# Kernel optimization log

Measured on AMD Instinct MI355X. Metric: run time of the kernel, lower is better.

Reference implementation:

```python
import jax, jax.numpy as jnp
import numpy as np

def _binarize(x):
    # sign-binarize: -1 where x<0 else +1 (matches tf.where(inputs<0,-1.0,1.0))
    return jnp.where(x < 0, -1.0, 1.0).astype(jnp.float32)

def setup_inputs() -> dict:
    key = jax.random.key(0)
    k1, k2 = jax.random.split(key)
    B, D_IN, D_OUT = 8192, 4096, 4096
    inputs = jax.random.normal(k1, (B, D_IN), dtype=jnp.float32)
    # build() initializes kernel with RandomNormal(stddev=0.1) then assigns its binarized
    # version; we store the pre-binarized values since call() re-binarizes anyway.
    kernel = 0.1 * jax.random.normal(k2, (D_IN, D_OUT), dtype=jnp.float32)
    bias = jnp.zeros((D_OUT,), dtype=jnp.float32)
    return {"inputs": inputs, "kernel": kernel, "bias": bias}

def reference(inputs, kernel, bias):
    bx = _binarize(inputs)          # [B, D_in] in {-1, +1}
    bw = _binarize(kernel)          # [D_in, D_out] in {-1, +1}
    out = bx @ bw + bias            # [B, D_out]
    return jnp.tanh(out)
```

## Files before the change

### kernel.cpp

```cpp
#include <hip/hip_runtime.h>


#define B_DIM 8192
#define K_DIM 4096
#define N_DIM 4096
#define BK 64
#define NT (K_DIM / BK)

typedef int   i32x4 __attribute__((ext_vector_type(4)));
typedef unsigned char u8;

__device__ __forceinline__ unsigned char binq8(float v) {
    return (v < 0.0f) ? 0xFFu : 0x01u;
}

__device__ __forceinline__ float fast_tanh(float x) {
    float ax = __builtin_fabsf(x);
    float t  = __expf(-2.0f * ax);
    float r  = (1.0f - t) * __builtin_amdgcn_rcpf(1.0f + t);
    return __builtin_copysignf(r, x);
}

__global__ __launch_bounds__(256) void binarize_a_kernel(
    const float* __restrict__ in, u8* __restrict__ out, long n16) {
    long i = (long)blockIdx.x * blockDim.x + threadIdx.x;
    const long stride = (long)gridDim.x * blockDim.x;
    for (; i < n16; i += stride) {
        const float4* p = (const float4*)in + 4 * i;
        float4 v0 = p[0], v1 = p[1], v2 = p[2], v3 = p[3];
        unsigned int w0 = (unsigned)binq8(v0.x) | ((unsigned)binq8(v0.y) << 8)
                        | ((unsigned)binq8(v0.z) << 16) | ((unsigned)binq8(v0.w) << 24);
        unsigned int w1 = (unsigned)binq8(v1.x) | ((unsigned)binq8(v1.y) << 8)
                        | ((unsigned)binq8(v1.z) << 16) | ((unsigned)binq8(v1.w) << 24);
        unsigned int w2 = (unsigned)binq8(v2.x) | ((unsigned)binq8(v2.y) << 8)
                        | ((unsigned)binq8(v2.z) << 16) | ((unsigned)binq8(v2.w) << 24);
        unsigned int w3 = (unsigned)binq8(v3.x) | ((unsigned)binq8(v3.y) << 8)
                        | ((unsigned)binq8(v3.z) << 16) | ((unsigned)binq8(v3.w) << 24);
        i32x4 o = {(int)w0, (int)w1, (int)w2, (int)w3};
        *(i32x4*)(out + i * 16) = o;
    }
}

__global__ __launch_bounds__(256) void bintrans_kernel(
    const float* __restrict__ W, u8* __restrict__ Bt) {
    __shared__ u8 tile[64][64];
    const int n0  = blockIdx.x * 64;
    const int k0  = blockIdx.y * 64;
    const int tid = threadIdx.x;
    const int r   = tid >> 4;
    const int c4  = (tid & 15) * 4;
#pragma unroll
    for (int i = 0; i < 4; ++i) {
        const int k = i * 16 + r;
        float4 v = *(const float4*)(W + (size_t)(k0 + k) * N_DIM + n0 + c4);
        unsigned int p = (unsigned)binq8(v.x) | ((unsigned)binq8(v.y) << 8)
                       | ((unsigned)binq8(v.z) << 16) | ((unsigned)binq8(v.w) << 24);
        *(unsigned int*)&tile[k][c4] = p;
    }
    __syncthreads();
    const int n  = tid >> 2;
    const int ks = (tid & 3) * 16;
    unsigned int o[4];
#pragma unroll
    for (int q = 0; q < 4; ++q) {
        unsigned int p = 0;
#pragma unroll
        for (int j = 0; j < 4; ++j)
            p |= (unsigned)tile[ks + q * 4 + j][n] << (8 * j);
        o[q] = p;
    }
    i32x4 ov = {(int)o[0], (int)o[1], (int)o[2], (int)o[3]};
    *(i32x4*)(Bt + (size_t)(n0 + n) * K_DIM + k0 + ks) = ov;
}

__global__ __launch_bounds__(512, 2) void bgemm_kernel(
    const u8* __restrict__ A,
    const u8* __restrict__ Bt,
    const float* __restrict__ bias,
    float* __restrict__ C) {

    __shared__ __align__(1024) char lds[131072];

    const int tid = threadIdx.x;
    const int l   = tid & 63;
    const int w   = tid >> 6;
    const int wr  = w >> 2;
    const int wc  = w & 3;

    const int wg  = blockIdx.x;
    const int per = gridDim.x >> 3;
    const int swz = (wg & 7) * per + (wg >> 3);
    const int NBN = N_DIM / 256;
    const int bm  = swz / NBN;
    const int bn  = swz % NBN;

    const int sslot = (tid & 3) ^ ((tid >> 3) & 3);
    const u8* A0 = A  + (size_t)(bm * 256 + (tid >> 2)) * K_DIM + sslot * 16;
    const u8* B0 = Bt + (size_t)(bn * 256 + (tid >> 2)) * K_DIM + sslot * 16;
    const int ldsA_st = w * 1024;
    const int ldsB_st = 16384 + w * 1024;

    const int colb = ((l >> 4) ^ ((l >> 1) & 3)) << 4;
    const int aoff = (wr * 128 + (l & 15)) * 64 + colb;
    const int boff = 16384 + (wc * 64 + (l & 15)) * 64 + colb;

#define GLL(srcp, ldsoff)                                                        \
    __builtin_amdgcn_global_load_lds(                                            \
        (const __attribute__((address_space(1))) void*)(srcp),                   \
        (__attribute__((address_space(3))) void*)(lds + (ldsoff)), 16, 0, 0)

    i32x4 acc[8][4];
#pragma unroll
    for (int mf = 0; mf < 8; ++mf)
#pragma unroll
        for (int nf = 0; nf < 4; ++nf) acc[mf][nf] = (i32x4){0, 0, 0, 0};

#pragma unroll
    for (int tp = 0; tp < 3; ++tp) {
        const int db = tp << 15;
        const int kk = tp * BK;
        GLL(A0 + kk,                          db + ldsA_st);
        GLL(A0 + (size_t)128 * K_DIM + kk,    db + ldsA_st + 8192);
        GLL(B0 + kk,                          db + ldsB_st);
        GLL(B0 + (size_t)128 * K_DIM + kk,    db + ldsB_st + 8192);
    }
    asm volatile("s_waitcnt vmcnt(8)" ::: "memory");
    __builtin_amdgcn_s_barrier();

    for (int t = 0; t < NT; ++t) {
        const int cur = (t & 3) << 15;
        const int db  = ((t + 3) & 3) << 15;
        const int tp  = (t + 3 < NT) ? (t + 3) : 0;
        const int kk  = tp * BK;

        i32x4 a[4], b[4];

        GLL(A0 + kk,                       db + ldsA_st);
        GLL(A0 + (size_t)128 * K_DIM + kk, db + ldsA_st + 8192);
#pragma unroll
        for (int nf = 0; nf < 4; ++nf)
            b[nf] = *(const i32x4*)(lds + cur + boff + nf * 1024);
#pragma unroll
        for (int mf = 0; mf < 4; ++mf)
            a[mf] = *(const i32x4*)(lds + cur + aoff + mf * 1024);
        __builtin_amdgcn_s_barrier();
        asm volatile("s_waitcnt lgkmcnt(0)" ::: "memory");
        __builtin_amdgcn_sched_barrier(0);
        __builtin_amdgcn_s_setprio(1);
#pragma unroll
        for (int mf = 0; mf < 4; ++mf)
#pragma unroll
            for (int nf = 0; nf < 4; ++nf)
                acc[mf][nf] = __builtin_amdgcn_mfma_i32_16x16x64_i8(
                    a[mf], b[nf], acc[mf][nf], 0, 0, 0);
        __builtin_amdgcn_s_setprio(0);
        __builtin_amdgcn_s_barrier();

        GLL(B0 + kk,                       db + ldsB_st);
        GLL(B0 + (size_t)128 * K_DIM + kk, db + ldsB_st + 8192);
#pragma unroll
        for (int mf = 0; mf < 4; ++mf)
            a[mf] = *(const i32x4*)(lds + cur + aoff + 4096 + mf * 1024);
        __builtin_amdgcn_s_barrier();
        asm volatile("s_waitcnt lgkmcnt(0)" ::: "memory");
        __builtin_amdgcn_sched_barrier(0);
        __builtin_amdgcn_s_setprio(1);
#pragma unroll
        for (int mf = 0; mf < 4; ++mf)
#pragma unroll
            for (int nf = 0; nf < 4; ++nf)
                acc[4 + mf][nf] = __builtin_amdgcn_mfma_i32_16x16x64_i8(
                    a[mf], b[nf], acc[4 + mf][nf], 0, 0, 0);
        __builtin_amdgcn_s_setprio(0);
        asm volatile("s_waitcnt vmcnt(8)" ::: "memory");
        __builtin_amdgcn_s_barrier();
    }

    const int cn  = l & 15;
    const int cr4 = (l >> 4) * 4;
    float bv[4];
#pragma unroll
    for (int nf = 0; nf < 4; ++nf)
        bv[nf] = bias[bn * 256 + wc * 64 + nf * 16 + cn];

#pragma unroll
    for (int mf = 0; mf < 8; ++mf) {
        const size_t row0 = (size_t)bm * 256 + wr * 128 + mf * 16 + cr4;
#pragma unroll
        for (int nf = 0; nf < 4; ++nf) {
            const size_t col = (size_t)bn * 256 + wc * 64 + nf * 16 + cn;
#pragma unroll
            for (int r = 0; r < 4; ++r)
                C[(row0 + r) * N_DIM + col] =
                    fast_tanh((float)acc[mf][nf][r] + bv[nf]);
        }
    }
#undef GLL
}

extern "C" void kernel_launch(void* const* d_in, const int* in_sizes, int n_in,
                              void* d_out, int out_size, void* d_ws, size_t ws_size,
                              hipStream_t stream) {
    const float* inputs = (const float*)d_in[0];
    const float* weight = (const float*)d_in[1];
    const float* bias   = (const float*)d_in[2];
    float* out = (float*)d_out;

    const size_t a_bytes = (size_t)B_DIM * K_DIM;
    const size_t b_bytes = (size_t)K_DIM * N_DIM;
    if (ws_size < a_bytes + b_bytes) return;

    u8* Abin = (u8*)d_ws;
    u8* Btb  = (u8*)((char*)d_ws + a_bytes);

    binarize_a_kernel<<<2048, 256, 0, stream>>>(inputs, Abin, (long)B_DIM * K_DIM / 16);

    dim3 tgrid(N_DIM / 64, K_DIM / 64);
    bintrans_kernel<<<tgrid, 256, 0, stream>>>(weight, Btb);

    bgemm_kernel<<<(B_DIM / 256) * (N_DIM / 256), 512, 0, stream>>>(Abin, Btb, bias, out);
}
```

Baseline: 394.0 us.

## Switch binary GEMM to FP4 operands with scaled 16x16x128 MFMA

Signs are now packed as 4-bit FP4 values (±1.0 encodings) rather than int8, halving the workspace and the global/LDS traffic for both operands. The GEMM uses the MX-scaled f8f6f4 MFMA in FP4 mode, with unit scales and float accumulation, so each instruction covers 128 K elements instead of 64. Half the tile loop iterations remain at the same tile shape. It relies on the FP4 encoding and zero-extended register packing matching the instruction's expected layout, and exact integer sums staying representable in fp32.

Measured after the change: 337.6 us. -14.3%, faster.

```diff
diff --git a/kernel.cpp b/kernel.cpp
--- a/kernel.cpp
+++ b/kernel.cpp
@@ -4,14 +4,17 @@
 #define B_DIM 8192
 #define K_DIM 4096
 #define N_DIM 4096
-#define BK 64
-#define NT (K_DIM / BK)
-
+#define KB    (K_DIM / 2)
+#define BKB   64
+#define NT    (K_DIM / 128)
+
+typedef float f32x4 __attribute__((ext_vector_type(4)));
 typedef int   i32x4 __attribute__((ext_vector_type(4)));
+typedef int   i32x8 __attribute__((ext_vector_type(8)));
 typedef unsigned char u8;
 
-__device__ __forceinline__ unsigned char binq8(float v) {
-    return (v < 0.0f) ? 0xFFu : 0x01u;
+__device__ __forceinline__ unsigned int nib4(float v) {
+    return (v < 0.0f) ? 0xAu : 0x2u;
 }
 
 __device__ __forceinline__ float fast_tanh(float x) {
@@ -22,21 +25,20 @@
 }
 
 __global__ __launch_bounds__(256) void binarize_a_kernel(
-    const float* __restrict__ in, u8* __restrict__ out, long n16) {
+    const float* __restrict__ in, u8* __restrict__ out, long n32) {
     long i = (long)blockIdx.x * blockDim.x + threadIdx.x;
     const long stride = (long)gridDim.x * blockDim.x;
-    for (; i < n16; i += stride) {
-        const float4* p = (const float4*)in + 4 * i;
-        float4 v0 = p[0], v1 = p[1], v2 = p[2], v3 = p[3];
-        unsigned int w0 = (unsigned)binq8(v0.x) | ((unsigned)binq8(v0.y) << 8)
-                        | ((unsigned)binq8(v0.z) << 16) | ((unsigned)binq8(v0.w) << 24);
-        unsigned int w1 = (unsigned)binq8(v1.x) | ((unsigned)binq8(v1.y) << 8)
-                        | ((unsigned)binq8(v1.z) << 16) | ((unsigned)binq8(v1.w) << 24);
-        unsigned int w2 = (unsigned)binq8(v2.x) | ((unsigned)binq8(v2.y) << 8)
-                        | ((unsigned)binq8(v2.z) << 16) | ((unsigned)binq8(v2.w) << 24);
-        unsigned int w3 = (unsigned)binq8(v3.x) | ((unsigned)binq8(v3.y) << 8)
-                        | ((unsigned)binq8(v3.z) << 16) | ((unsigned)binq8(v3.w) << 24);
-        i32x4 o = {(int)w0, (int)w1, (int)w2, (int)w3};
+    for (; i < n32; i += stride) {
+        const float4* p = (const float4*)in + 8 * i;
+        unsigned int w[4];
+#pragma unroll
+        for (int q = 0; q < 4; ++q) {
+            float4 a = p[2 * q], b = p[2 * q + 1];
+            w[q] = nib4(a.x)        | (nib4(a.y) << 4)  | (nib4(a.z) << 8)
+                 | (nib4(a.w) << 12)| (nib4(b.x) << 16) | (nib4(b.y) << 20)
+                 | (nib4(b.z) << 24)| (nib4(b.w) << 28);
+        }
+        i32x4 o = {(int)w[0], (int)w[1], (int)w[2], (int)w[3]};
         *(i32x4*)(out + i * 16) = o;
     }
 }
@@ -53,24 +55,20 @@
     for (int i = 0; i < 4; ++i) {
         const int k = i * 16 + r;
         float4 v = *(const float4*)(W + (size_t)(k0 + k) * N_DIM + n0 + c4);
-        unsigned int p = (unsigned)binq8(v.x) | ((unsigned)binq8(v.y) << 8)
-                       | ((unsigned)binq8(v.z) << 16) | ((unsigned)binq8(v.w) << 24);
+        unsigned int p = nib4(v.x) | (nib4(v.y) << 8) | (nib4(v.z) << 16)
+                       | (nib4(v.w) << 24);
         *(unsigned int*)&tile[k][c4] = p;
     }
     __syncthreads();
     const int n  = tid >> 2;
     const int ks = (tid & 3) * 16;
-    unsigned int o[4];
-#pragma unroll
-    for (int q = 0; q < 4; ++q) {
-        unsigned int p = 0;
-#pragma unroll
-        for (int j = 0; j < 4; ++j)
-            p |= (unsigned)tile[ks + q * 4 + j][n] << (8 * j);
-        o[q] = p;
-    }
-    i32x4 ov = {(int)o[0], (int)o[1], (int)o[2], (int)o[3]};
-    *(i32x4*)(Bt + (size_t)(n0 + n) * K_DIM + k0 + ks) = ov;
+    unsigned int lo = 0, hi = 0;
+#pragma unroll
+    for (int j = 0; j < 8; ++j) lo |= (unsigned)tile[ks + j][n]     << (4 * j);
+#pragma unroll
+    for (int j = 0; j < 8; ++j) hi |= (unsigned)tile[ks + 8 + j][n] << (4 * j);
+    uint2 o; o.x = lo; o.y = hi;
+    *(uint2*)(Bt + (size_t)(n0 + n) * KB + ((k0 + ks) >> 1)) = o;
 }
 
 __global__ __launch_bounds__(512, 2) void bgemm_kernel(
@@ -95,8 +93,8 @@
     const int bn  = swz % NBN;
 
     const int sslot = (tid & 3) ^ ((tid >> 3) & 3);
-    const u8* A0 = A  + (size_t)(bm * 256 + (tid >> 2)) * K_DIM + sslot * 16;
-    const u8* B0 = Bt + (size_t)(bn * 256 + (tid >> 2)) * K_DIM + sslot * 16;
+    const u8* A0 = A  + (size_t)(bm * 256 + (tid >> 2)) * KB + sslot * 16;
+    const u8* B0 = Bt + (size_t)(bn * 256 + (tid >> 2)) * KB + sslot * 16;
     const int ldsA_st = w * 1024;
     const int ldsB_st = 16384 + w * 1024;
 
@@ -109,20 +107,22 @@
         (const __attribute__((address_space(1))) void*)(srcp),                   \
         (__attribute__((address_space(3))) void*)(lds + (ldsoff)), 16, 0, 0)
 
-    i32x4 acc[8][4];
+    f32x4 acc[8][4];
 #pragma unroll
     for (int mf = 0; mf < 8; ++mf)
 #pragma unroll
-        for (int nf = 0; nf < 4; ++nf) acc[mf][nf] = (i32x4){0, 0, 0, 0};
+        for (int nf = 0; nf < 4; ++nf) acc[mf][nf] = (f32x4){0.f, 0.f, 0.f, 0.f};
+
+    const i32x4 z4 = {0, 0, 0, 0};
 
 #pragma unroll
     for (int tp = 0; tp < 3; ++tp) {
         const int db = tp << 15;
-        const int kk = tp * BK;
-        GLL(A0 + kk,                          db + ldsA_st);
-        GLL(A0 + (size_t)128 * K_DIM + kk,    db + ldsA_st + 8192);
-        GLL(B0 + kk,                          db + ldsB_st);
-        GLL(B0 + (size_t)128 * K_DIM + kk,    db + ldsB_st + 8192);
+        const int kk = tp * BKB;
+        GLL(A0 + kk,                       db + ldsA_st);
+        GLL(A0 + (size_t)128 * KB + kk,    db + ldsA_st + 8192);
+        GLL(B0 + kk,                       db + ldsB_st);
+        GLL(B0 + (size_t)128 * KB + kk,    db + ldsB_st + 8192);
     }
     asm volatile("s_waitcnt vmcnt(8)" ::: "memory");
     __builtin_amdgcn_s_barrier();
@@ -131,46 +131,60 @@
         const int cur = (t & 3) << 15;
         const int db  = ((t + 3) & 3) << 15;
         const int tp  = (t + 3 < NT) ? (t + 3) : 0;
-        const int kk  = tp * BK;
-
-        i32x4 a[4], b[4];
-
-        GLL(A0 + kk,                       db + ldsA_st);
-        GLL(A0 + (size_t)128 * K_DIM + kk, db + ldsA_st + 8192);
+        const int kk  = tp * BKB;
+
+        i32x4 at[4], bt[4];
+        i32x8 a8[4], b8[4];
+
+        GLL(A0 + kk,                    db + ldsA_st);
+        GLL(A0 + (size_t)128 * KB + kk, db + ldsA_st + 8192);
 #pragma unroll
         for (int nf = 0; nf < 4; ++nf)
-            b[nf] = *(const i32x4*)(lds + cur + boff + nf * 1024);
-#pragma unroll
-        for (int mf = 0; mf < 4; ++mf)
-            a[mf] = *(const i32x4*)(lds + cur + aoff + mf * 1024);
+            bt[nf] = *(const i32x4*)(lds + cur + boff + nf * 1024);
+#pragma unroll
+        for (int mf = 0; mf < 4; ++mf)
+            at[mf] = *(const i32x4*)(lds + cur + aoff + mf * 1024);
         __builtin_amdgcn_s_barrier();
         asm volatile("s_waitcnt lgkmcnt(0)" ::: "memory");
         __builtin_amdgcn_sched_barrier(0);
+#pragma unroll
+        for (int nf = 0; nf < 4; ++nf)
+            b8[nf] = __builtin_shufflevector(bt[nf], z4, 0, 1, 2, 3, 4, 5, 6, 7);
+#pragma unroll
+        for (int mf = 0; mf < 4; ++mf)
+            a8[mf] = __builtin_shufflevector(at[mf], z4, 0, 1, 2, 3, 4, 5, 6, 7);
         __builtin_amdgcn_s_setprio(1);
 #pragma unroll
         for (int mf = 0; mf < 4; ++mf)
 #pragma unroll
             for (int nf = 0; nf < 4; ++nf)
-                acc[mf][nf] = __builtin_amdgcn_mfma_i32_16x16x64_i8(
-                    a[mf], b[nf], acc[mf][nf], 0, 0, 0);
+                acc[mf][nf] = __builtin_amdgcn_mfma_scale_f32_16x16x128_f8f6f4(
+                    a8[mf], b8[nf], acc[mf][nf],
+                    4, 4,
+                    0, 0x7F7F7F7F,
+                    0, 0x7F7F7F7F);
         __builtin_amdgcn_s_setprio(0);
         __builtin_amdgcn_s_barrier();
 
-        GLL(B0 + kk,                       db + ldsB_st);
-        GLL(B0 + (size_t)128 * K_DIM + kk, db + ldsB_st + 8192);
-#pragma unroll
-        for (int mf = 0; mf < 4; ++mf)
-            a[mf] = *(const i32x4*)(lds + cur + aoff + 4096 + mf * 1024);
+        GLL(B0 + kk,                    db + ldsB_st);
+        GLL(B0 + (size_t)128 * KB + kk, db + ldsB_st + 8192);
+#pragma unroll
+        for (int mf = 0; mf < 4; ++mf)
+            at[mf] = *(const i32x4*)(lds + cur + aoff + 4096 + mf * 1024);
         __builtin_amdgcn_s_barrier();
         asm volatile("s_waitcnt lgkmcnt(0)" ::: "memory");
         __builtin_amdgcn_sched_barrier(0);
+#pragma unroll
+        for (int mf = 0; mf < 4; ++mf)
+            a8[mf] = __builtin_shufflevector(at[mf], z4, 0, 1, 2, 3, 4, 5, 6, 7);
         __builtin_amdgcn_s_setprio(1);
 #pragma unroll
         for (int mf = 0; mf < 4; ++mf)
 #pragma unroll
             for (int nf = 0; nf < 4; ++nf)
-                acc[4 + mf][nf] = __builtin_amdgcn_mfma_i32_16x16x64_i8(
-                    a[mf], b[nf], acc[4 + mf][nf], 0, 0, 0);
+                acc[4 + mf][nf] = __builtin_amdgcn_mfma_scale_f32_16x16x128_f8f6f4(
+                    a8[mf], b8[nf], acc[4 + mf][nf],
+                    4, 4, 0, 0x7F7F7F7F, 0, 0x7F7F7F7F);
         __builtin_amdgcn_s_setprio(0);
         asm volatile("s_waitcnt vmcnt(8)" ::: "memory");
         __builtin_amdgcn_s_barrier();
@@ -191,8 +205,7 @@
             const size_t col = (size_t)bn * 256 + wc * 64 + nf * 16 + cn;
 #pragma unroll
             for (int r = 0; r < 4; ++r)
-                C[(row0 + r) * N_DIM + col] =
-                    fast_tanh((float)acc[mf][nf][r] + bv[nf]);
+                C[(row0 + r) * N_DIM + col] = fast_tanh(acc[mf][nf][r] + bv[nf]);
         }
     }
 #undef GLL
@@ -206,14 +219,14 @@
     const float* bias   = (const float*)d_in[2];
     float* out = (float*)d_out;
 
-    const size_t a_bytes = (size_t)B_DIM * K_DIM;
-    const size_t b_bytes = (size_t)K_DIM * N_DIM;
+    const size_t a_bytes = (size_t)B_DIM * KB;
+    const size_t b_bytes = (size_t)N_DIM * KB;
     if (ws_size < a_bytes + b_bytes) return;
 
     u8* Abin = (u8*)d_ws;
     u8* Btb  = (u8*)((char*)d_ws + a_bytes);
 
-    binarize_a_kernel<<<2048, 256, 0, stream>>>(inputs, Abin, (long)B_DIM * K_DIM / 16);
+    binarize_a_kernel<<<2048, 256, 0, stream>>>(inputs, Abin, (long)B_DIM * K_DIM / 32);
 
     dim3 tgrid(N_DIM / 64, K_DIM / 64);
     bintrans_kernel<<<tgrid, 256, 0, stream>>>(weight, Btb);
```
